# Kernel tuning notes

Measured on AMD Instinct MI355X. Metric: run time of the kernel, lower is better.

The kernel has to match this reference:

```python
import jax, jax.numpy as jnp
import numpy as np

T = 4096          # time steps
I = 3             # input_size
R = 4096          # reservoir_size
LEAK = 0.1        # leaking_rate
RHO = 0.9         # spectral_radius
SPARSITY = 0.5


def setup_inputs() -> dict:
    key = jax.random.key(0)
    k1, k2, k3, k4 = jax.random.split(key, 4)
    x = jax.random.normal(k1, (T, I), dtype=jnp.float32)
    Win = jax.random.uniform(k2, (R, I), minval=-0.5, maxval=0.5, dtype=jnp.float32)
    Wh = jax.random.uniform(k3, (R, R), minval=-0.5, maxval=0.5, dtype=jnp.float32)
    mask = (jax.random.uniform(k4, (R, R)) < SPARSITY).astype(jnp.float32)
    Wh_np = np.asarray(Wh * mask, dtype=np.float64)
    # rescale to spectral radius RHO (power iteration estimate of dominant |eig|)
    v = np.random.default_rng(0).normal(size=R)
    rho = 1.0
    for _ in range(100):
        v = Wh_np @ v
        rho = np.linalg.norm(v)
        v = v / rho
    Wh = jnp.asarray(Wh_np * (RHO / rho), dtype=jnp.float32)
    return {"x": x, "Win": Win, "Wh": Wh}


def reference(x, Win, Wh):
    # Precompute all input projections in one GEMM: [T, R]
    ux = x @ Win.T

    def step(h, u):
        h_new = jnp.tanh(u + Wh @ h)
        h = LEAK * h + (1.0 - LEAK) * h_new
        return h, h

    h0 = jnp.zeros((Wh.shape[0],), dtype=x.dtype)
    _, hs = jax.lax.scan(step, h0, ux)   # hs: [T, R]
    return jnp.concatenate([hs, x], axis=1)  # H: [T, R + I]
```

## Files before the change

### kernel.cpp

```cpp
#include <hip/hip_runtime.h>
#include <cmath>


#define T_STEPS  4096
#define R_SIZE   4096
#define I_SIZE   3
#define OUT_COLS (R_SIZE + I_SIZE)
#define NB       256
#define BT       256
#define RPB      16
#define RPW      4
#define NREP     8
#define LEAK     0.1f

typedef _Float16 h2 __attribute__((ext_vector_type(2)));
typedef _Float16 h4 __attribute__((ext_vector_type(4)));
typedef _Float16 h8 __attribute__((ext_vector_type(8)));
typedef unsigned u32x4 __attribute__((ext_vector_type(4)));

__device__ __forceinline__ float fdot2f(h2 a, h2 b, float c) {
#if __has_builtin(__builtin_amdgcn_fdot2)
    return __builtin_amdgcn_fdot2(a, b, c, false);
#else
    return c + (float)a[0] * (float)b[0] + (float)a[1] * (float)b[1];
#endif
}

__device__ __forceinline__ float fast_tanhf(float s) {
    float av = __builtin_fabsf(s);
    float e  = __builtin_amdgcn_exp2f(-2.8853900817779268f * av);
    float r  = (1.0f - e) * __builtin_amdgcn_rcpf(1.0f + e);
    return __builtin_copysignf(r, s);
}

__device__ __forceinline__ void poll16(const unsigned* p0, const unsigned* p1,
                                       const unsigned* p2, const unsigned* p3,
                                       u32x4& a0, u32x4& a1, u32x4& a2, u32x4& a3) {
    asm volatile(
        "global_load_dwordx4 %0, %4, off sc0 sc1\n\t"
        "global_load_dwordx4 %1, %5, off sc0 sc1\n\t"
        "global_load_dwordx4 %2, %6, off sc0 sc1\n\t"
        "global_load_dwordx4 %3, %7, off sc0 sc1\n\t"
        "s_waitcnt vmcnt(0)"
        : "=&v"(a0), "=&v"(a1), "=&v"(a2), "=&v"(a3)
        : "v"(p0), "v"(p1), "v"(p2), "v"(p3)
        : "memory");
}

__device__ __forceinline__ _Float16 lo_half(unsigned w) {
    return __builtin_bit_cast(_Float16, (unsigned short)(w & 0xffffu));
}

__device__ __forceinline__ int check16(const u32x4& a0, const u32x4& a1,
                                       const u32x4& a2, const u32x4& a3,
                                       unsigned tg) {
    unsigned bad = ((a0[0] >> 16) ^ tg) | ((a0[1] >> 16) ^ tg) |
                   ((a0[2] >> 16) ^ tg) | ((a0[3] >> 16) ^ tg) |
                   ((a1[0] >> 16) ^ tg) | ((a1[1] >> 16) ^ tg) |
                   ((a1[2] >> 16) ^ tg) | ((a1[3] >> 16) ^ tg) |
                   ((a2[0] >> 16) ^ tg) | ((a2[1] >> 16) ^ tg) |
                   ((a2[2] >> 16) ^ tg) | ((a2[3] >> 16) ^ tg) |
                   ((a3[0] >> 16) ^ tg) | ((a3[1] >> 16) ^ tg) |
                   ((a3[2] >> 16) ^ tg) | ((a3[3] >> 16) ^ tg);
    return bad == 0u;
}

__global__ void __launch_bounds__(BT, 1) esn_kernel(
    const float* __restrict__ Wh,
    const float* __restrict__ Win,
    const float* __restrict__ x,
    float* __restrict__ out,
    unsigned* __restrict__ ex0,
    unsigned* __restrict__ ex1,
    unsigned rep_mask)
{
    __shared__ alignas(16) unsigned short hl[R_SIZE];
    __shared__ float xs[T_STEPS * I_SIZE];

    const int tid  = threadIdx.x;
    const int bid  = blockIdx.x;
    const int wv   = tid >> 6;
    const int lane = tid & 63;
    const int r0   = bid * RPB;

    h8 wreg[RPW * 8];
    #pragma unroll
    for (int rr = 0; rr < RPW; ++rr) {
        const float* src = Wh + (size_t)(r0 + wv * RPW + rr) * R_SIZE;
        #pragma unroll
        for (int j = 0; j < 8; ++j) {
            int e = (j * 64 + lane) * 8;
            float4 a = *(const float4*)(src + e);
            float4 b = *(const float4*)(src + e + 4);
            h8 hv;
            hv[0] = (_Float16)a.x; hv[1] = (_Float16)a.y;
            hv[2] = (_Float16)a.z; hv[3] = (_Float16)a.w;
            hv[4] = (_Float16)b.x; hv[5] = (_Float16)b.y;
            hv[6] = (_Float16)b.z; hv[7] = (_Float16)b.w;
            wreg[rr * 8 + j] = hv;
        }
    }

    for (int i = tid; i < T_STEPS * I_SIZE; i += BT) xs[i] = x[i];

    float win0 = 0.f, win1 = 0.f, win2 = 0.f;
    if (lane < RPW) {
        int r = r0 + wv * RPW + lane;
        win0 = Win[(size_t)r * I_SIZE + 0];
        win1 = Win[(size_t)r * I_SIZE + 1];
        win2 = Win[(size_t)r * I_SIZE + 2];
    }
    float hown = 0.0f;

    const unsigned rep  = (unsigned)bid & rep_mask;
    const unsigned nrep = rep_mask + 1u;
    const unsigned* pa[2][4];
    #pragma unroll
    for (int m = 0; m < 4; ++m) {
        pa[0][m] = ex0 + rep * R_SIZE + m * 1024 + tid * 4;
        pa[1][m] = ex1 + rep * R_SIZE + m * 1024 + tid * 4;
    }

    __syncthreads();

    unsigned long long tgt = 0;
    unsigned P = 0;

    for (int t = 0; t < T_STEPS; ++t) {
        const int par = t & 1;
        unsigned* __restrict__ exw = par ? ex0 : ex1;

        const float xt0 = xs[t * 3 + 0];
        const float xt1 = xs[t * 3 + 1];
        const float xt2 = xs[t * 3 + 2];

        __builtin_amdgcn_s_sleep(6);

        if (P) {
            for (int i = 0; i < 4096; ++i) {
                if (__builtin_amdgcn_s_memrealtime() >= tgt) break;
                __builtin_amdgcn_s_sleep(2);
            }
        }

        u32x4 a0, a1, a2, a3;
        const unsigned tg = (unsigned)t;
        poll16(pa[par][0], pa[par][1], pa[par][2], pa[par][3], a0, a1, a2, a3);
        int ok = check16(a0, a1, a2, a3, tg);
        const int missed = !__all(ok);
        if (missed) {
            do {
                __builtin_amdgcn_s_sleep(1);
                if (!ok) {
                    poll16(pa[par][0], pa[par][1], pa[par][2], pa[par][3],
                           a0, a1, a2, a3);
                    ok = check16(a0, a1, a2, a3, tg);
                }
            } while (!__all(ok));
        }

        {
            unsigned long long arr = __builtin_amdgcn_s_memrealtime();
            P = missed ? (P + 8u > 2048u ? 2048u : P + 8u)
                       : (P ? P - 1u : 0u);
            tgt = arr + P;
        }

        {
            u32x4 aa[4] = {a0, a1, a2, a3};
            #pragma unroll
            for (int m = 0; m < 4; ++m) {
                h4 hv;
                hv[0] = lo_half(aa[m][0]); hv[1] = lo_half(aa[m][1]);
                hv[2] = lo_half(aa[m][2]); hv[3] = lo_half(aa[m][3]);
                *(h4*)&hl[m * 1024 + tid * 4] = hv;
            }
        }
        __syncthreads();

        h8 hreg[8];
        const h8* hl8 = (const h8*)hl;
        #pragma unroll
        for (int j = 0; j < 8; ++j) hreg[j] = hl8[j * 64 + lane];
        __syncthreads();

        float acc[RPW];
        #pragma unroll
        for (int rr = 0; rr < RPW; ++rr) {
            float a = 0.0f;
            #pragma unroll
            for (int j = 0; j < 8; ++j) {
                h8 w8 = wreg[rr * 8 + j];
                h8 hh = hreg[j];
                a = fdot2f(__builtin_shufflevector(w8, w8, 0, 1),
                           __builtin_shufflevector(hh, hh, 0, 1), a);
                a = fdot2f(__builtin_shufflevector(w8, w8, 2, 3),
                           __builtin_shufflevector(hh, hh, 2, 3), a);
                a = fdot2f(__builtin_shufflevector(w8, w8, 4, 5),
                           __builtin_shufflevector(hh, hh, 4, 5), a);
                a = fdot2f(__builtin_shufflevector(w8, w8, 6, 7),
                           __builtin_shufflevector(hh, hh, 6, 7), a);
            }
            #pragma unroll
            for (int s = 32; s; s >>= 1) a += __shfl_xor(a, s, 64);
            acc[rr] = a;
        }

        float hv = 0.0f;
        unsigned word = 0;
        if (lane < RPW) {
            float a = (lane == 0) ? acc[0]
                    : (lane == 1) ? acc[1]
                    : (lane == 2) ? acc[2] : acc[3];
            float u  = xt0 * win0 + xt1 * win1 + xt2 * win2;
            float hn = fast_tanhf(u + a);
            hv = LEAK * hown + (1.0f - LEAK) * hn;
            hown = hv;
            word = ((unsigned)(t + 1) << 16) |
                   (unsigned)__builtin_bit_cast(unsigned short, (_Float16)hv);
        }
        unsigned w0 = __shfl(word, 0, 64);
        unsigned w1 = __shfl(word, 1, 64);
        unsigned w2 = __shfl(word, 2, 64);
        unsigned w3 = __shfl(word, 3, 64);
        if ((unsigned)lane < nrep) {
            u32x4 pw = {w0, w1, w2, w3};
            unsigned* dst = exw + (unsigned)lane * R_SIZE + r0 + wv * RPW;
            asm volatile("global_store_dwordx4 %0, %1, off sc0 sc1"
                         :: "v"(dst), "v"(pw) : "memory");
        }
        if (lane < RPW) {
            out[(size_t)t * OUT_COLS + (r0 + wv * RPW + lane)] = hv;
        }
    }
}

__global__ void copy_x_kernel(const float* __restrict__ x, float* __restrict__ out) {
    int i = blockIdx.x * blockDim.x + threadIdx.x;
    if (i < T_STEPS * I_SIZE) {
        int t = i / I_SIZE, c = i % I_SIZE;
        out[(size_t)t * OUT_COLS + R_SIZE + c] = x[i];
    }
}

extern "C" void kernel_launch(void* const* d_in, const int* in_sizes, int n_in,
                              void* d_out, int out_size, void* d_ws, size_t ws_size,
                              hipStream_t stream) {
    const float* x   = (const float*)d_in[0];
    const float* Win = (const float*)d_in[1];
    const float* Wh  = (const float*)d_in[2];
    float* out = (float*)d_out;

    size_t need8 = (size_t)2 * NREP * R_SIZE * sizeof(unsigned);
    unsigned nrep = (ws_size >= need8) ? NREP : 1u;
    unsigned rep_mask = nrep - 1u;
    unsigned* ex0 = (unsigned*)d_ws;
    unsigned* ex1 = ex0 + (size_t)nrep * R_SIZE;

    hipMemsetAsync(d_ws, 0, (size_t)2 * nrep * R_SIZE * sizeof(unsigned),
                   stream);

    copy_x_kernel<<<dim3((T_STEPS * I_SIZE + BT - 1) / BT), dim3(BT), 0, stream>>>(x, out);

    void* args[] = {(void*)&Wh, (void*)&Win, (void*)&x, (void*)&out,
                    (void*)&ex0, (void*)&ex1, (void*)&rep_mask};
    hipError_t e = hipLaunchCooperativeKernel((void*)esn_kernel, dim3(NB), dim3(BT),
                                              args, 0, stream);
    if (e != hipSuccess) {
        esn_kernel<<<dim3(NB), dim3(BT), 0, stream>>>(Wh, Win, x, out,
                                                      ex0, ex1, rep_mask);
    }
}
```

Measured before the change: 8.870 ms.

## Double exchange replicas, drop fixed sleep and second barrier, use perm for tag/unpack

Raises the number of replicated exchange buffers from 8 to 16 so fewer blocks poll each copy, which is meant to cut contention on shared cache lines. Also removes the unconditional s_sleep before polling and the trailing __syncthreads after the LDS read, relying on the double-buffered exchange to keep the hl array safe to overwrite. Tag checking and unpacking to fp16 now use byte-permute to handle two words at once. The adaptive backoff update moves to after the store and decays faster. Dropping the barrier could open an LDS write-after-read race between waves, and more replicas mean more store traffic per step.

```diff
diff --git a/kernel.cpp b/kernel.cpp
--- a/kernel.cpp
+++ b/kernel.cpp
@@ -10,12 +10,12 @@
 #define BT       256
 #define RPB      16
 #define RPW      4
-#define NREP     8
+#define NREP     16
 #define LEAK     0.1f
 
 typedef _Float16 h2 __attribute__((ext_vector_type(2)));
-typedef _Float16 h4 __attribute__((ext_vector_type(4)));
 typedef _Float16 h8 __attribute__((ext_vector_type(8)));
+typedef unsigned u32x2 __attribute__((ext_vector_type(2)));
 typedef unsigned u32x4 __attribute__((ext_vector_type(4)));
 
 __device__ __forceinline__ float fdot2f(h2 a, h2 b, float c) {
@@ -47,21 +47,16 @@
         : "memory");
 }
 
-__device__ __forceinline__ _Float16 lo_half(unsigned w) {
-    return __builtin_bit_cast(_Float16, (unsigned short)(w & 0xffffu));
-}
-
+__device__ __forceinline__ unsigned tagbad4(const u32x4& a, unsigned tg2) {
+    unsigned t01 = __builtin_amdgcn_perm(a[1], a[0], 0x07060302u) ^ tg2;
+    unsigned t23 = __builtin_amdgcn_perm(a[3], a[2], 0x07060302u) ^ tg2;
+    return t01 | t23;
+}
 __device__ __forceinline__ int check16(const u32x4& a0, const u32x4& a1,
                                        const u32x4& a2, const u32x4& a3,
-                                       unsigned tg) {
-    unsigned bad = ((a0[0] >> 16) ^ tg) | ((a0[1] >> 16) ^ tg) |
-                   ((a0[2] >> 16) ^ tg) | ((a0[3] >> 16) ^ tg) |
-                   ((a1[0] >> 16) ^ tg) | ((a1[1] >> 16) ^ tg) |
-                   ((a1[2] >> 16) ^ tg) | ((a1[3] >> 16) ^ tg) |
-                   ((a2[0] >> 16) ^ tg) | ((a2[1] >> 16) ^ tg) |
-                   ((a2[2] >> 16) ^ tg) | ((a2[3] >> 16) ^ tg) |
-                   ((a3[0] >> 16) ^ tg) | ((a3[1] >> 16) ^ tg) |
-                   ((a3[2] >> 16) ^ tg) | ((a3[3] >> 16) ^ tg);
+                                       unsigned tg2) {
+    unsigned bad = tagbad4(a0, tg2) | tagbad4(a1, tg2) |
+                   tagbad4(a2, tg2) | tagbad4(a3, tg2);
     return bad == 0u;
 }
 
@@ -130,11 +125,10 @@
         const int par = t & 1;
         unsigned* __restrict__ exw = par ? ex0 : ex1;
 
-        const float xt0 = xs[t * 3 + 0];
-        const float xt1 = xs[t * 3 + 1];
-        const float xt2 = xs[t * 3 + 2];
-
-        __builtin_amdgcn_s_sleep(6);
+        float u = 0.0f;
+        if (lane < RPW)
+            u = xs[t * 3 + 0] * win0 + xs[t * 3 + 1] * win1 +
+                xs[t * 3 + 2] * win2;
 
         if (P) {
             for (int i = 0; i < 4096; ++i) {
@@ -144,9 +138,9 @@
         }
 
         u32x4 a0, a1, a2, a3;
-        const unsigned tg = (unsigned)t;
+        const unsigned tg2 = (unsigned)t * 0x00010001u;
         poll16(pa[par][0], pa[par][1], pa[par][2], pa[par][3], a0, a1, a2, a3);
-        int ok = check16(a0, a1, a2, a3, tg);
+        int ok = check16(a0, a1, a2, a3, tg2);
         const int missed = !__all(ok);
         if (missed) {
             do {
@@ -154,26 +148,19 @@
                 if (!ok) {
                     poll16(pa[par][0], pa[par][1], pa[par][2], pa[par][3],
                            a0, a1, a2, a3);
-                    ok = check16(a0, a1, a2, a3, tg);
+                    ok = check16(a0, a1, a2, a3, tg2);
                 }
             } while (!__all(ok));
-        }
-
-        {
-            unsigned long long arr = __builtin_amdgcn_s_memrealtime();
-            P = missed ? (P + 8u > 2048u ? 2048u : P + 8u)
-                       : (P ? P - 1u : 0u);
-            tgt = arr + P;
         }
 
         {
             u32x4 aa[4] = {a0, a1, a2, a3};
             #pragma unroll
             for (int m = 0; m < 4; ++m) {
-                h4 hv;
-                hv[0] = lo_half(aa[m][0]); hv[1] = lo_half(aa[m][1]);
-                hv[2] = lo_half(aa[m][2]); hv[3] = lo_half(aa[m][3]);
-                *(h4*)&hl[m * 1024 + tid * 4] = hv;
+                u32x2 w;
+                w[0] = __builtin_amdgcn_perm(aa[m][1], aa[m][0], 0x05040100u);
+                w[1] = __builtin_amdgcn_perm(aa[m][3], aa[m][2], 0x05040100u);
+                *(u32x2*)&hl[m * 1024 + tid * 4] = w;
             }
         }
         __syncthreads();
@@ -182,7 +169,6 @@
         const h8* hl8 = (const h8*)hl;
         #pragma unroll
         for (int j = 0; j < 8; ++j) hreg[j] = hl8[j * 64 + lane];
-        __syncthreads();
 
         float acc[RPW];
         #pragma unroll
@@ -212,7 +198,6 @@
             float a = (lane == 0) ? acc[0]
                     : (lane == 1) ? acc[1]
                     : (lane == 2) ? acc[2] : acc[3];
-            float u  = xt0 * win0 + xt1 * win1 + xt2 * win2;
             float hn = fast_tanhf(u + a);
             hv = LEAK * hown + (1.0f - LEAK) * hn;
             hown = hv;
@@ -229,6 +214,14 @@
             asm volatile("global_store_dwordx4 %0, %1, off sc0 sc1"
                          :: "v"(dst), "v"(pw) : "memory");
         }
+
+        {
+            unsigned long long nowp = __builtin_amdgcn_s_memrealtime();
+            P = missed ? (P + 8u > 2048u ? 2048u : P + 8u)
+                       : (P >= 2u ? P - 2u : 0u);
+            tgt = nowp + P;
+        }
+
         if (lane < RPW) {
             out[(size_t)t * OUT_COLS + (r0 + wv * RPW + lane)] = hv;
         }
@@ -251,8 +244,9 @@
     const float* Wh  = (const float*)d_in[2];
     float* out = (float*)d_out;
 
-    size_t need8 = (size_t)2 * NREP * R_SIZE * sizeof(unsigned);
-    unsigned nrep = (ws_size >= need8) ? NREP : 1u;
+    size_t need16 = (size_t)2 * 16 * R_SIZE * sizeof(unsigned);
+    size_t need8  = (size_t)2 *  8 * R_SIZE * sizeof(unsigned);
+    unsigned nrep = (ws_size >= need16) ? 16u : (ws_size >= need8 ? 8u : 1u);
     unsigned rep_mask = nrep - 1u;
     unsigned* ex0 = (unsigned*)d_ws;
     unsigned* ex1 = ex0 + (size_t)nrep * R_SIZE;
```

Result: no change. 8.703 ms (-1.9%).
